# Performance work log

Hardware: AMD Instinct MI355X
Metric: run time of the kernel (lower is better)

The kernel has to match this reference:

```python
import jax, jax.numpy as jnp
import numpy as np

EMB_DIM = 1024
ATT_DIM = 1024

def setup_inputs() -> dict:
    key = jax.random.key(0)
    ks = jax.random.split(key, 7)
    B, S = 8, 2048
    x_h = jax.random.normal(ks[0], (B, S, EMB_DIM), dtype=jnp.float32)
    # Linear params (stored as [in, out] for x @ W + b)
    sq = 1.0 / np.sqrt(EMB_DIM)
    Wq = jax.random.uniform(ks[1], (EMB_DIM, ATT_DIM), jnp.float32, -sq, sq)
    bq = jax.random.uniform(ks[2], (ATT_DIM,), jnp.float32, -sq, sq)
    Wk = jax.random.uniform(ks[3], (EMB_DIM, ATT_DIM), jnp.float32, -sq, sq)
    bk = jax.random.uniform(ks[4], (ATT_DIM,), jnp.float32, -sq, sq)
    Wv = jax.random.uniform(ks[5], (EMB_DIM, EMB_DIM), jnp.float32, -sq, sq)
    bv = jax.random.uniform(ks[6], (EMB_DIM,), jnp.float32, -sq, sq)
    return {"x_h": x_h, "Wq": Wq, "bq": bq, "Wk": Wk, "bk": bk, "Wv": Wv, "bv": bv}

def reference(x_h, Wq, bq, Wk, bk, Wv, bv):
    q = x_h @ Wq + bq               # [B,S,att_dim]
    k = x_h @ Wk + bk               # [B,S,att_dim]
    v = x_h @ Wv + bv               # [B,S,emb_dim]
    scale = 1.0 / jnp.sqrt(jnp.asarray(k.shape[-1], q.dtype))
    scores = jnp.einsum('bqd,bkd->bqk', q, k) * scale   # [B,S,S]
    # NOTE: original softmaxes over dim=1 (the QUERY axis), not the key axis.
    attn = jax.nn.softmax(scores, axis=1)
    return jnp.einsum('bqk,bkd->bqd', attn, v)
```

## Files before the change

kernel.cpp:

```cpp
#include <hip/hip_runtime.h>
#include <math.h>

typedef __bf16 bf16x8 __attribute__((ext_vector_type(8)));
typedef float f32x4 __attribute__((ext_vector_type(4)));
typedef unsigned short ushort8 __attribute__((ext_vector_type(8)));
typedef unsigned short ushort4v __attribute__((ext_vector_type(4)));
typedef unsigned short u16;

#define DEVINL __device__ __forceinline__

DEVINL u16 f2bf(float f) {
    union { float f; unsigned u; } a; a.f = f;
    unsigned u = a.u;
    return (u16)((u + 0x7FFFu + ((u >> 16) & 1u)) >> 16);
}
DEVINL float bf2f(u16 h) { return __uint_as_float(((unsigned)h) << 16); }

DEVINL void gload_lds16(const void* g, void* l) {
    __builtin_amdgcn_global_load_lds(
        (__attribute__((address_space(1))) void*)(g),
        (__attribute__((address_space(3))) void*)(l),
        16, 0, 0);
}

template<int EPI>
__global__ __launch_bounds__(512, 2)
void gemm256(const u16* __restrict__ A, int lda, long sAz,
             const u16* __restrict__ B, int ldb, long sBz,
             void* __restrict__ Cv, int ldc, long sCz,
             const float* __restrict__ bias, float* __restrict__ part,
             float scale, int K)
{
    __shared__ u16 lds[65536];
    const int tid = threadIdx.x;

    const int nx = gridDim.x, ny = gridDim.y;
    const int nwg = nx * ny * gridDim.z;
    const int orig = blockIdx.x + nx * (blockIdx.y + ny * blockIdx.z);
    const int id = (orig & 7) * (nwg >> 3) + (orig >> 3);
    const int tile_x = id % nx;
    const int rem = id / nx;
    const int tile_y = rem % ny;
    const long bz = rem / ny;

    const u16* Ab = A + bz * sAz;
    const u16* Bb = B + bz * sBz;
    const int row0 = tile_x * 256, col0 = tile_y * 256;

    const int sr = tid >> 2;
    const int csw = ((tid & 3) * 16) ^ (((sr >> 1) & 3) << 4);
    const u16* Ag = Ab + (long)(row0 + sr) * lda + (csw >> 1);
    const u16* Bg = Bb + (long)(col0 + sr) * ldb + (csw >> 1);
    const int dst0 = tid * 8;

    const int lane = tid & 63, wid = tid >> 6;
    const int wm = wid >> 2, wn = wid & 3;
    const int lane_r = lane & 15;
    const int rdcol = (((lane >> 4) * 16) ^ (((lane_r >> 1) & 3) << 4)) >> 1;
    const int arow0 = wm * 128 + lane_r;
    const int brow0 = wn * 64 + lane_r;

    const int NT = K >> 6;
    f32x4 acc[8][4] = {};
    bf16x8 af[4], bfrag[4];

    auto issueA = [&](int t1, int s, int buf) {
        const u16* g = Ag + (long)t1 * 64 + s * 32;
        u16* d = &lds[(buf * 2 + s) * 8192 + dst0];
        gload_lds16(g, d);
        gload_lds16(g + (long)128 * lda, d + 4096);
    };
    auto issueB = [&](int t1, int s, int buf) {
        const u16* g = Bg + (long)t1 * 64 + s * 32;
        u16* d = &lds[32768 + (buf * 2 + s) * 8192 + dst0];
        gload_lds16(g, d);
        gload_lds16(g + (long)128 * ldb, d + 4096);
    };

#define READ_A(s, h)                                                        \
    _Pragma("unroll")                                                       \
    for (int m = 0; m < 4; ++m)                                             \
        af[m] = *(const bf16x8*)&lds[(buf * 2 + (s)) * 8192 +               \
                     (arow0 + (h) * 64 + m * 16) * 32 + rdcol];

#define READ_B(s)                                                           \
    _Pragma("unroll")                                                       \
    for (int n = 0; n < 4; ++n)                                             \
        bfrag[n] = *(const bf16x8*)&lds[32768 + (buf * 2 + (s)) * 8192 +    \
                     (brow0 + n * 16) * 32 + rdcol];

#define MFMA16(h)                                                           \
    __builtin_amdgcn_s_setprio(1);                                          \
    _Pragma("unroll")                                                       \
    for (int m = 0; m < 4; ++m)                                             \
        _Pragma("unroll")                                                   \
        for (int n = 0; n < 4; ++n)                                         \
            acc[(h) * 4 + m][n] = __builtin_amdgcn_mfma_f32_16x16x32_bf16(  \
                bfrag[n], af[m], acc[(h) * 4 + m][n], 0, 0, 0);             \
    __builtin_amdgcn_s_setprio(0);

    issueA(0, 0, 0); issueB(0, 0, 0); issueA(0, 1, 0); issueB(0, 1, 0);
    asm volatile("s_waitcnt vmcnt(4)" ::: "memory");
    __builtin_amdgcn_s_barrier();

    for (int t = 0; t < NT - 1; ++t) {
        const int buf = t & 1, nbuf = buf ^ 1;
        READ_A(0, 0); READ_B(0);
        issueA(t + 1, 0, nbuf);
        __builtin_amdgcn_s_barrier();
        MFMA16(0);
        __builtin_amdgcn_s_barrier();
        READ_A(0, 1);
        issueB(t + 1, 0, nbuf);
        asm volatile("s_waitcnt vmcnt(4)" ::: "memory");
        __builtin_amdgcn_s_barrier();
        MFMA16(1);
        __builtin_amdgcn_s_barrier();
        READ_A(1, 0); READ_B(1);
        issueA(t + 1, 1, nbuf);
        __builtin_amdgcn_s_barrier();
        MFMA16(0);
        __builtin_amdgcn_s_barrier();
        READ_A(1, 1);
        issueB(t + 1, 1, nbuf);
        asm volatile("s_waitcnt vmcnt(4)" ::: "memory");
        __builtin_amdgcn_s_barrier();
        MFMA16(1);
        __builtin_amdgcn_s_barrier();
    }
    {
        const int buf = (NT - 1) & 1;
        READ_A(0, 0); READ_B(0);
        __builtin_amdgcn_s_barrier();
        MFMA16(0);
        __builtin_amdgcn_s_barrier();
        READ_A(0, 1);
        asm volatile("s_waitcnt vmcnt(0)" ::: "memory");
        __builtin_amdgcn_s_barrier();
        MFMA16(1);
        __builtin_amdgcn_s_barrier();
        READ_A(1, 0); READ_B(1);
        __builtin_amdgcn_s_barrier();
        MFMA16(0);
        __builtin_amdgcn_s_barrier();
        READ_A(1, 1);
        __builtin_amdgcn_s_barrier();
        MFMA16(1);
    }
#undef READ_A
#undef READ_B
#undef MFMA16

    const int erow = lane & 15, ecol0 = (lane >> 4) * 4;
    float4 bias4[4];
    if constexpr (EPI == 0) {
#pragma unroll
        for (int nf = 0; nf < 4; ++nf)
            bias4[nf] = *(const float4*)&bias[col0 + wn * 64 + nf * 16 + ecol0];
    }
    f32x4 csum[4] = {};
#pragma unroll
    for (int mf = 0; mf < 8; ++mf) {
        const int gr = row0 + wm * 128 + mf * 16 + erow;
#pragma unroll
        for (int nf = 0; nf < 4; ++nf) {
            const int gc = col0 + wn * 64 + nf * 16 + ecol0;
            f32x4 v = acc[mf][nf];
            if constexpr (EPI == 0) {
                v[0] += bias4[nf].x; v[1] += bias4[nf].y;
                v[2] += bias4[nf].z; v[3] += bias4[nf].w;
                ushort4v o = { f2bf(v[0]), f2bf(v[1]), f2bf(v[2]), f2bf(v[3]) };
                *(ushort4v*)((u16*)Cv + bz * sCz + (long)gr * ldc + gc) = o;
            } else if constexpr (EPI == 1) {
                f32x4 e;
#pragma unroll
                for (int r = 0; r < 4; ++r) e[r] = __expf(v[r] * scale);
                csum[0] += 0.0f;
                csum[nf] += e;
                ushort4v o = { f2bf(e[0]), f2bf(e[1]), f2bf(e[2]), f2bf(e[3]) };
                *(ushort4v*)((u16*)Cv + bz * sCz + (long)gr * ldc + gc) = o;
            } else {
                *(float4*)((float*)Cv + bz * sCz + (long)gr * ldc + gc) =
                    make_float4(v[0], v[1], v[2], v[3]);
            }
        }
    }
    if constexpr (EPI == 1) {
#pragma unroll
        for (int nf = 0; nf < 4; ++nf)
#pragma unroll
            for (int r = 0; r < 4; ++r) {
                float s = csum[nf][r];
                s += __shfl_xor(s, 1);
                s += __shfl_xor(s, 2);
                s += __shfl_xor(s, 4);
                s += __shfl_xor(s, 8);
                csum[nf][r] = s;
            }
        if ((lane & 15) == 0) {
#pragma unroll
            for (int nf = 0; nf < 4; ++nf) {
                float* p = part + ((bz * 16 + (long)tile_x * 2 + wm) * 2048)
                         + col0 + wn * 64 + nf * 16 + ecol0;
                *(float4*)p = make_float4(csum[nf][0], csum[nf][1],
                                          csum[nf][2], csum[nf][3]);
            }
        }
    }
}

__global__ void cast_x_k(const float* __restrict__ x, u16* __restrict__ o)
{
    const int i = blockIdx.x * 256 + threadIdx.x;
    const float4* xv = (const float4*)x;
    const float4 a = xv[(long)i * 2], b = xv[(long)i * 2 + 1];
    ushort8 r;
    r[0] = f2bf(a.x); r[1] = f2bf(a.y); r[2] = f2bf(a.z); r[3] = f2bf(a.w);
    r[4] = f2bf(b.x); r[5] = f2bf(b.y); r[6] = f2bf(b.z); r[7] = f2bf(b.w);
    *(ushort8*)(o + (long)i * 8) = r;
}

__global__ void wt_k(const float* __restrict__ Wq, const float* __restrict__ Wk,
                     const float* __restrict__ Wv, u16* __restrict__ Wt)
{
    __shared__ float t[32][33];
    const int z = blockIdx.z;
    const float* W = (z == 0) ? Wq : ((z == 1) ? Wk : Wv);
    const int k0 = blockIdx.x * 32, n0 = blockIdx.y * 32;
    const int tx = threadIdx.x, ty = threadIdx.y;
#pragma unroll
    for (int j = 0; j < 32; j += 8)
        t[ty + j][tx] = W[(long)(k0 + ty + j) * 1024 + n0 + tx];
    __syncthreads();
#pragma unroll
    for (int j = 0; j < 32; j += 8)
        Wt[((long)z * 1024 + n0 + ty + j) * 1024 + k0 + tx] = f2bf(t[tx][ty + j]);
}

__global__ void bias_k(const float* __restrict__ bq, const float* __restrict__ bk,
                       const float* __restrict__ bv, float* __restrict__ bcat)
{
    const int i = blockIdx.x * 256 + threadIdx.x;
    bcat[i] = (i < 1024) ? bq[i] : ((i < 2048) ? bk[i - 1024] : bv[i - 2048]);
}

__global__ void rcp_k(const float* __restrict__ part, float* __restrict__ rden)
{
    const int b = blockIdx.y;
    const int k = blockIdx.x * 256 + threadIdx.x;
    float s = 0.f;
#pragma unroll
    for (int c = 0; c < 16; ++c) s += part[((long)b * 16 + c) * 2048 + k];
    rden[b * 2048 + k] = 1.0f / s;
}

__global__ void vt_k(const u16* __restrict__ qkv, const float* __restrict__ rden,
                     u16* __restrict__ Vt)
{
    __shared__ float t[32][33];
    const int b = blockIdx.z;
    const int k0 = blockIdx.x * 32, d0 = blockIdx.y * 32;
    const int tx = threadIdx.x, ty = threadIdx.y;
#pragma unroll
    for (int j = 0; j < 32; j += 8) {
        const int k = k0 + ty + j;
        t[ty + j][tx] = bf2f(qkv[((long)b * 2048 + k) * 3072 + 2048 + d0 + tx])
                        * rden[b * 2048 + k];
    }
    __syncthreads();
#pragma unroll
    for (int j = 0; j < 32; j += 8)
        Vt[((long)b * 1024 + d0 + ty + j) * 2048 + k0 + tx] = f2bf(t[tx][ty + j]);
}

extern "C" void kernel_launch(void* const* d_in, const int* in_sizes, int n_in,
                              void* d_out, int out_size, void* d_ws, size_t ws_size,
                              hipStream_t stream)
{
    const float* x  = (const float*)d_in[0];
    const float* Wq = (const float*)d_in[1];
    const float* bq = (const float*)d_in[2];
    const float* Wk = (const float*)d_in[3];
    const float* bk = (const float*)d_in[4];
    const float* Wv = (const float*)d_in[5];
    const float* bv = (const float*)d_in[6];

    char* ws = (char*)d_ws;
    u16*   qkv  = (u16*)(ws);
    u16*   E    = (u16*)(ws + 100663296);
    u16*   Vt   = (u16*)(ws + 167772160);
    u16*   xb   = (u16*)(ws + 201326592);
    u16*   Wt   = (u16*)(ws + 234881024);
    float* bcat = (float*)(ws + 241172480);
    float* part = (float*)(ws + 241184768);
    float* rden = (float*)(ws + 243281920);

    const long sQKV = (long)2048 * 3072;
    const long sE   = (long)2048 * 2048;
    const long sVt  = (long)1024 * 2048;
    const long sO   = (long)2048 * 1024;

    cast_x_k<<<8192, 256, 0, stream>>>(x, xb);
    wt_k<<<dim3(32, 32, 3), dim3(32, 8), 0, stream>>>(Wq, Wk, Wv, Wt);
    bias_k<<<12, 256, 0, stream>>>(bq, bk, bv, bcat);
    gemm256<0><<<dim3(64, 12, 1), 512, 0, stream>>>(
        xb, 1024, 0, Wt, 1024, 0, qkv, 3072, 0, bcat, nullptr, 0.f, 1024);
    gemm256<1><<<dim3(8, 8, 8), 512, 0, stream>>>(
        qkv, 3072, sQKV, qkv + 1024, 3072, sQKV, E, 2048, sE,
        nullptr, part, 0.03125f, 1024);
    rcp_k<<<dim3(8, 8), 256, 0, stream>>>(part, rden);
    vt_k<<<dim3(64, 32, 8), dim3(32, 8), 0, stream>>>(qkv, rden, Vt);
    gemm256<2><<<dim3(8, 4, 8), 512, 0, stream>>>(
        E, 2048, sE, Vt, 2048, sVt, d_out, 1024, sO,
        nullptr, nullptr, 1.f, 2048);
}
```

Before: 304.4 us.

## Cut GEMM main-loop barriers to two per tile and drop XCD tile remap

Replaces the barrier pairs around every MFMA block in the bf16 GEMM main loop with a single combined vmcnt wait plus barrier after each half-K step, leaving two barriers per iteration instead of eight. The aim is to stop waves stalling at workgroup barriers so LDS reads, global-to-LDS loads and MFMAs can interleave more freely. It also removes the block-index remap that spread tiles across XCDs and uses blockIdx directly, which may change L2 locality and scheduling. A redundant accumulate of zero in the exp epilogue is dropped. The main risk is an LDS race if a wave reads a buffer before the others' loads into it have landed.

```diff
diff --git a/kernel.cpp b/kernel.cpp
--- a/kernel.cpp
+++ b/kernel.cpp
@@ -33,15 +33,8 @@
 {
     __shared__ u16 lds[65536];
     const int tid = threadIdx.x;
-
-    const int nx = gridDim.x, ny = gridDim.y;
-    const int nwg = nx * ny * gridDim.z;
-    const int orig = blockIdx.x + nx * (blockIdx.y + ny * blockIdx.z);
-    const int id = (orig & 7) * (nwg >> 3) + (orig >> 3);
-    const int tile_x = id % nx;
-    const int rem = id / nx;
-    const int tile_y = rem % ny;
-    const long bz = rem / ny;
+    const int tile_x = blockIdx.x, tile_y = blockIdx.y;
+    const long bz = blockIdx.z;
 
     const u16* Ab = A + bz * sAz;
     const u16* Bb = B + bz * sBz;
@@ -99,57 +92,46 @@
                 bfrag[n], af[m], acc[(h) * 4 + m][n], 0, 0, 0);             \
     __builtin_amdgcn_s_setprio(0);
 
+#define GATE(n)                                                             \
+    asm volatile("s_waitcnt vmcnt(" #n ")" ::: "memory");                   \
+    __builtin_amdgcn_s_barrier();
+
     issueA(0, 0, 0); issueB(0, 0, 0); issueA(0, 1, 0); issueB(0, 1, 0);
-    asm volatile("s_waitcnt vmcnt(4)" ::: "memory");
-    __builtin_amdgcn_s_barrier();
+    GATE(4);
 
     for (int t = 0; t < NT - 1; ++t) {
         const int buf = t & 1, nbuf = buf ^ 1;
         READ_A(0, 0); READ_B(0);
         issueA(t + 1, 0, nbuf);
-        __builtin_amdgcn_s_barrier();
-        MFMA16(0);
-        __builtin_amdgcn_s_barrier();
+        MFMA16(0);
         READ_A(0, 1);
         issueB(t + 1, 0, nbuf);
-        asm volatile("s_waitcnt vmcnt(4)" ::: "memory");
-        __builtin_amdgcn_s_barrier();
-        MFMA16(1);
-        __builtin_amdgcn_s_barrier();
+        MFMA16(1);
+        GATE(4);
         READ_A(1, 0); READ_B(1);
         issueA(t + 1, 1, nbuf);
-        __builtin_amdgcn_s_barrier();
-        MFMA16(0);
-        __builtin_amdgcn_s_barrier();
+        MFMA16(0);
         READ_A(1, 1);
         issueB(t + 1, 1, nbuf);
-        asm volatile("s_waitcnt vmcnt(4)" ::: "memory");
-        __builtin_amdgcn_s_barrier();
-        MFMA16(1);
-        __builtin_amdgcn_s_barrier();
+        MFMA16(1);
+        GATE(4);
     }
     {
         const int buf = (NT - 1) & 1;
         READ_A(0, 0); READ_B(0);
-        __builtin_amdgcn_s_barrier();
-        MFMA16(0);
-        __builtin_amdgcn_s_barrier();
+        MFMA16(0);
         READ_A(0, 1);
-        asm volatile("s_waitcnt vmcnt(0)" ::: "memory");
-        __builtin_amdgcn_s_barrier();
-        MFMA16(1);
-        __builtin_amdgcn_s_barrier();
+        MFMA16(1);
+        GATE(0);
         READ_A(1, 0); READ_B(1);
-        __builtin_amdgcn_s_barrier();
-        MFMA16(0);
-        __builtin_amdgcn_s_barrier();
+        MFMA16(0);
         READ_A(1, 1);
-        __builtin_amdgcn_s_barrier();
         MFMA16(1);
     }
 #undef READ_A
 #undef READ_B
 #undef MFMA16
+#undef GATE
 
     const int erow = lane & 15, ecol0 = (lane >> 4) * 4;
     float4 bias4[4];
@@ -175,7 +157,6 @@
                 f32x4 e;
 #pragma unroll
                 for (int r = 0; r < 4; ++r) e[r] = __expf(v[r] * scale);
-                csum[0] += 0.0f;
                 csum[nf] += e;
                 ushort4v o = { f2bf(e[0]), f2bf(e[1]), f2bf(e[2]), f2bf(e[3]) };
                 *(ushort4v*)((u16*)Cv + bz * sCz + (long)gr * ldc + gc) = o;
```

Result: no change. 303.7 us (-0.2%).
